# Kernel optimization log

Hardware: AMD Instinct MI355X
Metric: run time of the kernel (lower is better)

## Reference

```python
import jax, jax.numpy as jnp
import numpy as np


def setup_inputs() -> dict:
    key = jax.random.key(0)
    k1, k2, k3, k4 = jax.random.split(key, 4)
    B, T, C, H = 4, 4096, 1024, 64
    x = jax.random.normal(k1, (B, T, C), dtype=jnp.float32)
    # nn.Linear weights, stored as (in, out) for x @ W
    s = 1.0 / np.sqrt(C)
    Wk = jax.random.uniform(k2, (C, H), dtype=jnp.float32, minval=-s, maxval=s)
    Wq = jax.random.uniform(k3, (C, H), dtype=jnp.float32, minval=-s, maxval=s)
    Wv = jax.random.uniform(k4, (C, H), dtype=jnp.float32, minval=-s, maxval=s)
    return {"x": x, "Wk": Wk, "Wq": Wq, "Wv": Wv}


def reference(x, Wk, Wq, Wv):
    # single-head causal self-attention (dropout=0 / eval mode)
    B, T, C = x.shape
    k = x @ Wk  # [B,T,H]
    q = x @ Wq  # [B,T,H]
    v = x @ Wv  # [B,T,H]
    scale = k.shape[-1] ** -0.5
    wei = jnp.einsum('bth,bsh->bts', q, k) * scale  # [B,T,T]
    causal = jnp.tril(jnp.ones((T, T), dtype=bool))
    wei = jnp.where(causal, wei, -jnp.inf)
    wei = jax.nn.softmax(wei, axis=-1)
    out = jnp.einsum('bts,bsh->bth', wei, v)  # [B,T,H]
    return out
```

## Files before the change

kernel.cpp:

```cpp
#include <hip/hip_runtime.h>
#include <hip/hip_bf16.h>

#define B_ 4
#define T_ 4096
#define C_ 1024
#define H_ 64
#define M_ (B_ * T_)
#define UPB 272

typedef __bf16 bf16x8 __attribute__((ext_vector_type(8)));
typedef float f32x8 __attribute__((ext_vector_type(8)));
typedef float f32x4 __attribute__((ext_vector_type(4)));
typedef unsigned short us8 __attribute__((ext_vector_type(8)));
typedef unsigned short us4 __attribute__((ext_vector_type(4)));

#define QSCALE 0.18033688011112042f
#define OFF2   23.083120654223414f

__device__ __forceinline__ unsigned short f2bf(float x) {
    return __builtin_bit_cast(unsigned short, (__bf16)x);
}
__device__ __forceinline__ float bf2f(unsigned short u) {
    return __builtin_bit_cast(float, (unsigned)u << 16);
}
__device__ __forceinline__ f32x4 mfma16(bf16x8 a, bf16x8 b, f32x4 c) {
    return __builtin_amdgcn_mfma_f32_16x16x32_bf16(a, b, c, 0, 0, 0);
}
__device__ __forceinline__ bf16x8 ldb8(const unsigned short* p) {
    return __builtin_bit_cast(bf16x8, *reinterpret_cast<const us8*>(p));
}
__device__ __forceinline__ bf16x8 ldlds8(const char* p) {
    return __builtin_bit_cast(bf16x8, *reinterpret_cast<const us8*>(p));
}
__device__ __forceinline__ void gll16(const void* g, char* ldsdst) {
    __builtin_amdgcn_global_load_lds(
        (const __attribute__((address_space(1))) unsigned*)g,
        (__attribute__((address_space(3))) unsigned*)ldsdst, 16, 0, 0);
}

__global__ __launch_bounds__(256) void wt_kernel(const float* __restrict__ Wk,
                                                 const float* __restrict__ Wq,
                                                 const float* __restrict__ Wv,
                                                 unsigned short* __restrict__ Wt) {
    __shared__ float t[64][65];
    const int wid = blockIdx.x >> 4;
    const int kb = (blockIdx.x & 15) * 64;
    const float* W = (wid == 0) ? Wk : (wid == 1 ? Wq : Wv);
    const int ty = threadIdx.x >> 6;
    const int tx = threadIdx.x & 63;
#pragma unroll
    for (int i = 0; i < 16; ++i) {
        int kl = i * 4 + ty;
        t[kl][tx] = W[(size_t)(kb + kl) * H_ + tx];
    }
    __syncthreads();
#pragma unroll
    for (int i = 0; i < 16; ++i) {
        int hl = i * 4 + ty;
        Wt[(size_t)(wid * 64 + hl) * C_ + kb + tx] = f2bf(t[tx][hl]);
    }
}

__global__ __launch_bounds__(256) void proj_kernel(const float* __restrict__ x,
                                                   const unsigned short* __restrict__ Wt,
                                                   unsigned short* __restrict__ Kb,
                                                   unsigned short* __restrict__ Qb,
                                                   unsigned short* __restrict__ Vt) {
    __shared__ char lds[61440];
    const int tid = threadIdx.x;
    const int w = tid >> 6, l = tid & 63;
    const int lg = l >> 4, cl = l & 15;
    const int mbase = blockIdx.x * 64;
    const int w64 = w << 6;

    f32x4 acc[12];
#pragma unroll
    for (int i = 0; i < 12; ++i) acc[i] = (f32x4){0.f, 0.f, 0.f, 0.f};

#define STAGE(AO, BO, KC)                                                        \
    {                                                                            \
        _Pragma("unroll") for (int i = 0; i < 2; ++i) {                          \
            int unit = i * 256 + tid;                                            \
            int row = unit >> 3, up = unit & 7;                                  \
            int lu = up ^ (row & 7);                                             \
            gll16(x + (size_t)(mbase + row) * C_ + (KC) + lu * 4,                \
                  lds + (AO) + (unsigned)(i * 256 + w64) * 16);                  \
        }                                                                        \
        _Pragma("unroll") for (int i = 0; i < 3; ++i) {                          \
            int unit = i * 256 + tid;                                            \
            int pr = unit >> 3, up = unit & 7;                                   \
            int u = up ^ (pr & 7);                                               \
            int r = pr * 2 + (u >> 2);                                           \
            gll16(Wt + (size_t)r * C_ + (KC) + (u & 3) * 8,                      \
                  lds + (BO) + (unsigned)(i * 256 + w64) * 16);                  \
        }                                                                        \
    }

#define COMPUTE(AO, BO)                                                          \
    {                                                                            \
        const int arow = w * 16 + cl;                                            \
        const int asw = cl & 7;                                                  \
        f32x4 alo = *reinterpret_cast<const f32x4*>(                             \
            lds + (AO) + arow * 128 + ((lg * 2) ^ asw) * 16);                    \
        f32x4 ahi = *reinterpret_cast<const f32x4*>(                             \
            lds + (AO) + arow * 128 + ((lg * 2 + 1) ^ asw) * 16);                \
        f32x8 af;                                                                \
        af[0] = alo[0]; af[1] = alo[1]; af[2] = alo[2]; af[3] = alo[3];          \
        af[4] = ahi[0]; af[5] = ahi[1]; af[6] = ahi[2]; af[7] = ahi[3];          \
        bf16x8 a = __builtin_convertvector(af, bf16x8);                          \
        _Pragma("unroll") for (int nf = 0; nf < 12; ++nf) {                      \
            int r = nf * 16 + cl;                                                \
            int pr = r >> 1;                                                     \
            bf16x8 bb = __builtin_bit_cast(bf16x8,                               \
                *reinterpret_cast<const us8*>(                                   \
                    lds + (BO) + pr * 128 +                                      \
                    ((((cl & 1) << 2) + lg) ^ (pr & 7)) * 16));                  \
            acc[nf] = mfma16(a, bb, acc[nf]);                                    \
        }                                                                        \
    }

    int a0 = 0, a1 = 8192, a2 = 16384;
    int b0 = 24576, b1 = 36864, b2 = 49152;

    STAGE(a0, b0, 0);
    STAGE(a1, b1, 32);
    for (int t = 0; t < 30; ++t) {
        asm volatile("s_waitcnt vmcnt(5)" ::: "memory");
        asm volatile("s_barrier" ::: "memory");
        STAGE(a2, b2, (t + 2) * 32);
        COMPUTE(a0, b0);
        int ta = a0; a0 = a1; a1 = a2; a2 = ta;
        int tb = b0; b0 = b1; b1 = b2; b2 = tb;
    }
    asm volatile("s_waitcnt vmcnt(5)" ::: "memory");
    asm volatile("s_barrier" ::: "memory");
    COMPUTE(a0, b0);
    asm volatile("s_waitcnt vmcnt(0)" ::: "memory");
    asm volatile("s_barrier" ::: "memory");
    COMPUTE(a1, b1);
#undef STAGE
#undef COMPUTE

    const int rbase = mbase + w * 16 + lg * 4;
#pragma unroll
    for (int nf = 0; nf < 12; ++nf) {
        int colg = nf * 16 + cl;
#pragma unroll
        for (int r = 0; r < 4; ++r) {
            float v = acc[nf][r];
            int m = rbase + r;
            if (colg < 64) {
                Kb[m * H_ + colg] = f2bf(v);
            } else if (colg < 128) {
                Qb[m * H_ + (colg - 64)] = f2bf(v * QSCALE);
            } else {
                int b = m >> 12, t = m & 4095, h = colg - 128;
                Vt[((b << 6) + h) * T_ + t] = f2bf(v);
            }
        }
    }
}

__global__ __launch_bounds__(256, 2) void attn_kernel(const unsigned short* __restrict__ Qb,
                                                      const unsigned short* __restrict__ Kb,
                                                      const unsigned short* __restrict__ Vt,
                                                      float* __restrict__ out,
                                                      unsigned short* __restrict__ Opart,
                                                      float* __restrict__ lpart) {
    __shared__ char lds[49152];
    const int tid = threadIdx.x;
    const int w = tid >> 6, l = tid & 63;
    const int lg = l >> 4, cl = l & 15;
    const int kgrp = lg * 8;
    char* pb = lds + 32768 + w * 4096;

    const int lin = blockIdx.x;
    const int xcd = lin & 7;
    const int b = xcd >> 1;
    const int f = (xcd & 1) * 136 + (lin >> 3);

    int qt = 0, Sp = 0;
    while (f >= Sp + ((qt + 2) >> 1)) { Sp += (qt + 2) >> 1; ++qt; }
    const int chunk = f - Sp;
    const int nc = (qt + 2) >> 1;

    const int qbase = qt * 128;
    const int qw = qbase + w * 32;
    const int s0 = chunk * 256;
    int s1 = s0 + 256;
    if (s1 > qbase + 128) s1 = qbase + 128;
    const int ntile = (s1 - s0) >> 6;

    const unsigned short* q0 = Qb + (size_t)(b * T_ + qw + cl) * H_;
    bf16x8 qa00 = ldb8(q0 + kgrp), qa01 = ldb8(q0 + 32 + kgrp);
    bf16x8 qa10 = ldb8(q0 + 16 * H_ + kgrp), qa11 = ldb8(q0 + 16 * H_ + 32 + kgrp);

    f32x4 o[2][4];
#pragma unroll
    for (int rf = 0; rf < 2; ++rf)
#pragma unroll
        for (int nf = 0; nf < 4; ++nf) o[rf][nf] = (f32x4){0.f, 0.f, 0.f, 0.f};
    float lrow[2][4] = {{0.f, 0.f, 0.f, 0.f}, {0.f, 0.f, 0.f, 0.f}};

#define STG(KO, VO, SB)                                                          \
    {                                                                            \
        _Pragma("unroll") for (int i = 0; i < 2; ++i) {                          \
            int u = i * 256 + tid;                                               \
            int row = u >> 3, up = u & 7;                                        \
            int lu = up ^ (row & 7);                                             \
            gll16(Kb + (size_t)(b * T_ + (SB) + row) * H_ + lu * 8,              \
                  lds + (KO) + (unsigned)(i * 256 + (w << 6)) * 16);             \
            gll16(Vt + (size_t)((b << 6) + row) * T_ + (SB) + lu * 8,            \
                  lds + (VO) + (unsigned)(i * 256 + (w << 6)) * 16);             \
        }                                                                        \
    }

    int k0o = 0, k1o = 8192;
    int v0o = 16384, v1o = 24576;

    STG(k0o, v0o, s0);
    for (int t = 0; t < ntile; ++t) {
        const int sbase = s0 + t * 64;
        asm volatile("s_waitcnt vmcnt(0)" ::: "memory");
        asm volatile("s_barrier" ::: "memory");
        if (t + 1 < ntile) STG(k1o, v1o, sbase + 64);

        if (qw + 31 >= sbase) {
            const bool diag = (sbase + 63 > qw);
            f32x4 sA[4], sB[4];
            __builtin_amdgcn_s_setprio(1);
#pragma unroll
            for (int nf = 0; nf < 4; ++nf) {
                const int row = nf * 16 + cl, sw = row & 7;
                bf16x8 k0v = ldlds8(lds + k0o + row * 128 + (lg ^ sw) * 16);
                bf16x8 k1v = ldlds8(lds + k0o + row * 128 + ((4 + lg) ^ sw) * 16);
                f32x4 z = (f32x4){0.f, 0.f, 0.f, 0.f};
                sA[nf] = mfma16(qa01, k1v, mfma16(qa00, k0v, z));
                sB[nf] = mfma16(qa11, k1v, mfma16(qa10, k0v, z));
            }
            __builtin_amdgcn_s_setprio(0);
#pragma unroll
            for (int nf = 0; nf < 4; ++nf) {
                const int col = sbase + nf * 16 + cl;
#pragma unroll
                for (int r = 0; r < 4; ++r) {
                    const int row = lg * 4 + r;
                    const int rowA = qw + row;
                    float pA = (diag && col > rowA)      ? 0.f : exp2f(sA[nf][r] - OFF2);
                    float pB = (diag && col > rowA + 16) ? 0.f : exp2f(sB[nf][r] - OFF2);
                    lrow[0][r] += pA;
                    lrow[1][r] += pB;
                    const int swz = (row & 7) << 4;
                    int lin0 = row * 128 + (nf * 16 + cl) * 2;
                    int lin1 = (16 + row) * 128 + (nf * 16 + cl) * 2;
                    *(unsigned short*)(pb + (lin0 ^ swz)) = f2bf(pA);
                    *(unsigned short*)(pb + (lin1 ^ swz)) = f2bf(pB);
                }
            }
            const int msk = (cl & 7) << 4;
            bf16x8 pa00 = ldlds8(pb + ((cl * 128 + lg * 16) ^ msk));
            bf16x8 pa01 = ldlds8(pb + ((cl * 128 + 64 + lg * 16) ^ msk));
            bf16x8 pa10 = ldlds8(pb + (((16 + cl) * 128 + lg * 16) ^ msk));
            bf16x8 pa11 = ldlds8(pb + (((16 + cl) * 128 + 64 + lg * 16) ^ msk));
            __builtin_amdgcn_s_setprio(1);
#pragma unroll
            for (int nf = 0; nf < 4; ++nf) {
                const int row = nf * 16 + cl, sw = row & 7;
                bf16x8 v0 = ldlds8(lds + v0o + row * 128 + (lg ^ sw) * 16);
                bf16x8 v1 = ldlds8(lds + v0o + row * 128 + ((4 + lg) ^ sw) * 16);
                o[0][nf] = mfma16(pa01, v1, mfma16(pa00, v0, o[0][nf]));
                o[1][nf] = mfma16(pa11, v1, mfma16(pa10, v0, o[1][nf]));
            }
            __builtin_amdgcn_s_setprio(0);
        }
        int tk = k0o; k0o = k1o; k1o = tk;
        int tv = v0o; v0o = v1o; v1o = tv;
    }
#undef STG

#pragma unroll
    for (int o16 = 1; o16 < 16; o16 <<= 1)
#pragma unroll
        for (int rf = 0; rf < 2; ++rf)
#pragma unroll
            for (int r = 0; r < 4; ++r)
                lrow[rf][r] += __shfl_xor(lrow[rf][r], o16);

    if (nc == 1) {
#pragma unroll
        for (int rf = 0; rf < 2; ++rf) {
            float inv[4];
#pragma unroll
            for (int r = 0; r < 4; ++r) inv[r] = 1.0f / lrow[rf][r];
#pragma unroll
            for (int nf = 0; nf < 4; ++nf)
#pragma unroll
                for (int r = 0; r < 4; ++r) {
                    int t = qw + rf * 16 + lg * 4 + r;
                    out[(size_t)(b * T_ + t) * H_ + nf * 16 + cl] =
                        o[rf][nf][r] * inv[r];
                }
        }
    } else {
        const int slot = b * UPB + f;
        unsigned short* Ob = Opart + (size_t)slot * 8192;
#pragma unroll
        for (int rf = 0; rf < 2; ++rf)
#pragma unroll
            for (int nf = 0; nf < 4; ++nf) {
                us4 v;
#pragma unroll
                for (int r = 0; r < 4; ++r) v[r] = f2bf(o[rf][nf][r]);
                *reinterpret_cast<us4*>(Ob + ((w * 8 + rf * 4 + nf) * 64 + l) * 4) = v;
            }
        if (cl == 0) {
#pragma unroll
            for (int rf = 0; rf < 2; ++rf)
#pragma unroll
                for (int r = 0; r < 4; ++r)
                    lpart[slot * 128 + w * 32 + rf * 16 + lg * 4 + r] = lrow[rf][r];
        }
    }
}

__global__ __launch_bounds__(256) void combine_kernel(const unsigned short* __restrict__ Opart,
                                                      const float* __restrict__ lpart,
                                                      float* __restrict__ out) {
    const int qt = 2 + blockIdx.x;
    const int b = blockIdx.y;
    const int c = (qt + 2) >> 1;
    const int slot0 = b * UPB + ((qt + 1) * (qt + 1)) / 4;

    const int p = blockIdx.z * 4 + (threadIdx.x >> 6);
    const int l = threadIdx.x & 63;
    const int wq = p >> 3, rf = (p >> 2) & 1, nf = p & 3;
    const int lg = l >> 4, cl = l & 15;

    float a[4] = {0.f, 0.f, 0.f, 0.f};
    float ls[4] = {0.f, 0.f, 0.f, 0.f};
    for (int j = 0; j < c; ++j) {
        const unsigned short* src =
            Opart + (size_t)(slot0 + j) * 8192 + (p * 64 + l) * 4;
        us4 v = *reinterpret_cast<const us4*>(src);
        const float* lp = lpart + (slot0 + j) * 128 + wq * 32 + rf * 16 + lg * 4;
#pragma unroll
        for (int e = 0; e < 4; ++e) {
            a[e] += bf2f(v[e]);
            ls[e] += lp[e];
        }
    }
#pragma unroll
    for (int e = 0; e < 4; ++e) {
        int row = qt * 128 + wq * 32 + rf * 16 + lg * 4 + e;
        out[(size_t)(b * T_ + row) * H_ + nf * 16 + cl] = a[e] / ls[e];
    }
}

extern "C" void kernel_launch(void* const* d_in, const int* in_sizes, int n_in,
                              void* d_out, int out_size, void* d_ws, size_t ws_size,
                              hipStream_t stream) {
    const float* x  = (const float*)d_in[0];
    const float* Wk = (const float*)d_in[1];
    const float* Wq = (const float*)d_in[2];
    const float* Wv = (const float*)d_in[3];
    float* out = (float*)d_out;

    char* ws = (char*)d_ws;
    unsigned short* Kb = (unsigned short*)(ws);
    unsigned short* Qb = (unsigned short*)(ws + 2097152);
    unsigned short* Vt = (unsigned short*)(ws + 2 * 2097152);
    unsigned short* Wt = (unsigned short*)(ws + 3 * 2097152);
    const size_t base = 6684672ull;
    unsigned short* Opart = (unsigned short*)(ws + base);
    float* lpart = (float*)(ws + base + (size_t)B_ * UPB * 16384);

    wt_kernel<<<dim3(48), dim3(256), 0, stream>>>(Wk, Wq, Wv, Wt);
    proj_kernel<<<dim3(256), dim3(256), 0, stream>>>(x, Wt, Kb, Qb, Vt);
    attn_kernel<<<dim3(8 * 136), dim3(256), 0, stream>>>(
        Qb, Kb, Vt, out, Opart, lpart);
    combine_kernel<<<dim3(30, B_, 8), dim3(256), 0, stream>>>(Opart, lpart, out);
}
```

Baseline: 61.96 us.

## Halve projection row tile and split output columns across waves

The projection kernel now processes 32 rows per block instead of 64, and launches 512 blocks instead of 256. The four waves are arranged as 2 row halves by 2 column halves, with 6 MFMA accumulators per wave instead of 12. A and B tiles share one LDS buffer per stage. The goal is more blocks to fill the CUs and fewer registers per wave. The cost is that each block loads the full W tile for half as many rows, which doubles the weight traffic per output row.

```diff
diff --git a/kernel.cpp b/kernel.cpp
--- a/kernel.cpp
+++ b/kernel.cpp
@@ -66,85 +66,83 @@
                                                    unsigned short* __restrict__ Kb,
                                                    unsigned short* __restrict__ Qb,
                                                    unsigned short* __restrict__ Vt) {
-    __shared__ char lds[61440];
+    __shared__ char lds[49152];
     const int tid = threadIdx.x;
     const int w = tid >> 6, l = tid & 63;
     const int lg = l >> 4, cl = l & 15;
-    const int mbase = blockIdx.x * 64;
-    const int w64 = w << 6;
-
-    f32x4 acc[12];
-#pragma unroll
-    for (int i = 0; i < 12; ++i) acc[i] = (f32x4){0.f, 0.f, 0.f, 0.f};
-
-#define STAGE(AO, BO, KC)                                                        \
+    const int rh = w & 1;
+    const int ch = w >> 1;
+    const int mbase = blockIdx.x * 32;
+
+    f32x4 acc[6];
+#pragma unroll
+    for (int i = 0; i < 6; ++i) acc[i] = (f32x4){0.f, 0.f, 0.f, 0.f};
+
+#define STAGE(BUF, KC)                                                           \
     {                                                                            \
-        _Pragma("unroll") for (int i = 0; i < 2; ++i) {                          \
-            int unit = i * 256 + tid;                                            \
-            int row = unit >> 3, up = unit & 7;                                  \
+        {                                                                        \
+            int row = tid >> 3, up = tid & 7;                                    \
             int lu = up ^ (row & 7);                                             \
             gll16(x + (size_t)(mbase + row) * C_ + (KC) + lu * 4,                \
-                  lds + (AO) + (unsigned)(i * 256 + w64) * 16);                  \
+                  lds + (BUF) + (unsigned)((w << 6)) * 16);                      \
         }                                                                        \
         _Pragma("unroll") for (int i = 0; i < 3; ++i) {                          \
-            int unit = i * 256 + tid;                                            \
-            int pr = unit >> 3, up = unit & 7;                                   \
-            int u = up ^ (pr & 7);                                               \
-            int r = pr * 2 + (u >> 2);                                           \
-            gll16(Wt + (size_t)r * C_ + (KC) + (u & 3) * 8,                      \
-                  lds + (BO) + (unsigned)(i * 256 + w64) * 16);                  \
+            int u = i * 256 + tid;                                               \
+            int pr = u >> 3, up = u & 7;                                         \
+            int uu = up ^ (pr & 7);                                              \
+            int r = pr * 2 + (uu >> 2);                                          \
+            gll16(Wt + (size_t)r * C_ + (KC) + (uu & 3) * 8,                     \
+                  lds + (BUF) + 4096 + (unsigned)(i * 256 + (w << 6)) * 16);     \
         }                                                                        \
     }
 
-#define COMPUTE(AO, BO)                                                          \
+#define COMPUTE(BUF)                                                             \
     {                                                                            \
-        const int arow = w * 16 + cl;                                            \
+        const int arow = rh * 16 + cl;                                           \
         const int asw = cl & 7;                                                  \
         f32x4 alo = *reinterpret_cast<const f32x4*>(                             \
-            lds + (AO) + arow * 128 + ((lg * 2) ^ asw) * 16);                    \
+            lds + (BUF) + arow * 128 + ((lg * 2) ^ asw) * 16);                   \
         f32x4 ahi = *reinterpret_cast<const f32x4*>(                             \
-            lds + (AO) + arow * 128 + ((lg * 2 + 1) ^ asw) * 16);                \
+            lds + (BUF) + arow * 128 + ((lg * 2 + 1) ^ asw) * 16);               \
         f32x8 af;                                                                \
         af[0] = alo[0]; af[1] = alo[1]; af[2] = alo[2]; af[3] = alo[3];          \
         af[4] = ahi[0]; af[5] = ahi[1]; af[6] = ahi[2]; af[7] = ahi[3];          \
         bf16x8 a = __builtin_convertvector(af, bf16x8);                          \
-        _Pragma("unroll") for (int nf = 0; nf < 12; ++nf) {                      \
-            int r = nf * 16 + cl;                                                \
+        _Pragma("unroll") for (int nf = 0; nf < 6; ++nf) {                       \
+            int r = ch * 96 + nf * 16 + cl;                                      \
             int pr = r >> 1;                                                     \
             bf16x8 bb = __builtin_bit_cast(bf16x8,                               \
                 *reinterpret_cast<const us8*>(                                   \
-                    lds + (BO) + pr * 128 +                                      \
+                    lds + (BUF) + 4096 + pr * 128 +                              \
                     ((((cl & 1) << 2) + lg) ^ (pr & 7)) * 16));                  \
             acc[nf] = mfma16(a, bb, acc[nf]);                                    \
         }                                                                        \
     }
 
-    int a0 = 0, a1 = 8192, a2 = 16384;
-    int b0 = 24576, b1 = 36864, b2 = 49152;
-
-    STAGE(a0, b0, 0);
-    STAGE(a1, b1, 32);
+    int u0 = 0, u1 = 16384, u2 = 32768;
+
+    STAGE(u0, 0);
+    STAGE(u1, 32);
     for (int t = 0; t < 30; ++t) {
-        asm volatile("s_waitcnt vmcnt(5)" ::: "memory");
+        asm volatile("s_waitcnt vmcnt(4)" ::: "memory");
         asm volatile("s_barrier" ::: "memory");
-        STAGE(a2, b2, (t + 2) * 32);
-        COMPUTE(a0, b0);
-        int ta = a0; a0 = a1; a1 = a2; a2 = ta;
-        int tb = b0; b0 = b1; b1 = b2; b2 = tb;
-    }
-    asm volatile("s_waitcnt vmcnt(5)" ::: "memory");
+        STAGE(u2, (t + 2) * 32);
+        COMPUTE(u0);
+        int tu = u0; u0 = u1; u1 = u2; u2 = tu;
+    }
+    asm volatile("s_waitcnt vmcnt(4)" ::: "memory");
     asm volatile("s_barrier" ::: "memory");
-    COMPUTE(a0, b0);
+    COMPUTE(u0);
     asm volatile("s_waitcnt vmcnt(0)" ::: "memory");
     asm volatile("s_barrier" ::: "memory");
-    COMPUTE(a1, b1);
+    COMPUTE(u1);
 #undef STAGE
 #undef COMPUTE
 
-    const int rbase = mbase + w * 16 + lg * 4;
-#pragma unroll
-    for (int nf = 0; nf < 12; ++nf) {
-        int colg = nf * 16 + cl;
+    const int rbase = mbase + rh * 16 + lg * 4;
+#pragma unroll
+    for (int nf = 0; nf < 6; ++nf) {
+        int colg = ch * 96 + nf * 16 + cl;
 #pragma unroll
         for (int r = 0; r < 4; ++r) {
             float v = acc[nf][r];
@@ -375,7 +373,7 @@
     float* lpart = (float*)(ws + base + (size_t)B_ * UPB * 16384);
 
     wt_kernel<<<dim3(48), dim3(256), 0, stream>>>(Wk, Wq, Wv, Wt);
-    proj_kernel<<<dim3(256), dim3(256), 0, stream>>>(x, Wt, Kb, Qb, Vt);
+    proj_kernel<<<dim3(512), dim3(256), 0, stream>>>(x, Wt, Kb, Qb, Vt);
     attn_kernel<<<dim3(8 * 136), dim3(256), 0, stream>>>(
         Qb, Kb, Vt, out, Opart, lpart);
     combine_kernel<<<dim3(30, B_, 8), dim3(256), 0, stream>>>(Opart, lpart, out);
```

New measurement: 64.37 us. +3.9%, slower.
